# Kernel optimization log

Hardware: AMD Instinct MI355X
Metric: run time of the kernel (lower is better)

The kernel has to match this reference:

```python
import jax, jax.numpy as jnp
import numpy as np

NUM_HEADS = 8
LN_EPS = 1e-6


def _layer_norm(x, gamma, beta):
    mu = jnp.mean(x, axis=-1, keepdims=True)
    var = jnp.mean(jnp.square(x - mu), axis=-1, keepdims=True)
    return (x - mu) / jnp.sqrt(var + LN_EPS) * gamma + beta


def setup_inputs() -> dict:
    key = jax.random.key(0)
    B, S, H, F = 4, 2048, 1024, 4096
    ks = jax.random.split(key, 12)
    scale = 1.0 / np.sqrt(H)
    x = jax.random.normal(ks[0], (B, S, H), dtype=jnp.float32)
    # additive padding mask: 1 where masked, 0 where attended
    mask = jax.random.randint(ks[1], (B, 1, 1, S), 0, 2).astype(jnp.float32)
    Wq = jax.random.normal(ks[2], (H, H), dtype=jnp.float32) * scale
    Wk = jax.random.normal(ks[3], (H, H), dtype=jnp.float32) * scale
    Wv = jax.random.normal(ks[4], (H, H), dtype=jnp.float32) * scale
    Wo = jax.random.normal(ks[5], (H, H), dtype=jnp.float32) * scale
    W1 = jax.random.normal(ks[6], (H, F), dtype=jnp.float32) * scale
    b1 = jnp.zeros((F,), dtype=jnp.float32)
    W2 = jax.random.normal(ks[7], (F, H), dtype=jnp.float32) * (1.0 / np.sqrt(F))
    b2 = jnp.zeros((H,), dtype=jnp.float32)
    gamma = jnp.ones((H,), dtype=jnp.float32)
    beta = jnp.zeros((H,), dtype=jnp.float32)
    return {"x": x, "mask": mask, "Wq": Wq, "Wk": Wk, "Wv": Wv, "Wo": Wo,
            "W1": W1, "b1": b1, "W2": W2, "b2": b2, "gamma": gamma, "beta": beta}


def reference(x, mask, Wq, Wk, Wv, Wo, W1, b1, W2, b2, gamma, beta):
    B, S, H = x.shape
    nh = NUM_HEADS
    d = H // nh

    def split_heads(t):
        return t.reshape(B, S, nh, d).transpose(0, 2, 1, 3)  # [B,nh,S,d]

    q = split_heads(x @ Wq)
    k = split_heads(x @ Wk)
    v = split_heads(x @ Wv)

    # FAITHFUL to source bug: score /= d**(-0.5)  ==  score * sqrt(d)
    scores = jnp.einsum('bhqd,bhkd->bhqk', q, k) * jnp.sqrt(jnp.float32(d))
    scores = scores + mask * (-1e9)
    attn = jax.nn.softmax(scores, axis=-1)
    ctx = jnp.einsum('bhqk,bhkd->bhqd', attn, v)
    ctx = ctx.transpose(0, 2, 1, 3).reshape(B, S, H)
    attn_out = ctx @ Wo

    # dropout = identity (eval mode)
    x = _layer_norm(x + attn_out, gamma, beta)
    ffn = jnp.maximum(x @ W1 + b1, 0.0) @ W2 + b2
    x = _layer_norm(x + ffn, gamma, beta)
    return x
```

## Files before the change

kernel.cpp:

```cpp
#include <hip/hip_runtime.h>


typedef __bf16 bf16;
typedef __bf16 bf16x4 __attribute__((ext_vector_type(4)));
typedef __bf16 bf16x8 __attribute__((ext_vector_type(8)));
typedef float  f32x4  __attribute__((ext_vector_type(4)));

#define MFMA16(a, b, c) __builtin_amdgcn_mfma_f32_16x16x32_bf16(a, b, c, 0, 0, 0)

typedef const __attribute__((address_space(1))) void* gas_cptr;
typedef __attribute__((address_space(3))) void* las_ptr;

__device__ __forceinline__ void g2l16(const void* g, void* l) {
    __builtin_amdgcn_global_load_lds((gas_cptr)g, (las_ptr)l, 16, 0, 0);
}

__device__ __forceinline__ uint b16bits(bf16 v) {
    union { bf16 h; unsigned short u; } cv; cv.h = v; return (uint)cv.u;
}

__device__ __forceinline__ int xcd_swz(int d, int nwg) {
    return (d & 7) * (nwg >> 3) + (d >> 3);
}

__global__ __launch_bounds__(256) void split_f32_k(
    const float* __restrict__ in, bf16* __restrict__ hi, bf16* __restrict__ lo)
{
    const long i = (long)blockIdx.x * 256 + threadIdx.x;
    const float4 v = *(const float4*)(in + i * 4);
    const float a[4] = {v.x, v.y, v.z, v.w};
    bf16x4 h, l;
#pragma unroll
    for (int j = 0; j < 4; j++) {
        h[j] = (bf16)a[j];
        l[j] = (bf16)(a[j] - (float)h[j]);
    }
    *(bf16x4*)(hi + i * 4) = h;
    *(bf16x4*)(lo + i * 4) = l;
}

__global__ __launch_bounds__(256) void mask_scan_k(
    const float* __restrict__ mask, unsigned short* __restrict__ cidx,
    int* __restrict__ nbuf)
{
    __shared__ int wsum[4];
    const int b = blockIdx.x, t = threadIdx.x;
    const int lane = t & 63, w = t >> 6;
    float m[8];
    *(float4*)&m[0] = *(const float4*)(mask + b * 2048 + t * 8);
    *(float4*)&m[4] = *(const float4*)(mask + b * 2048 + t * 8 + 4);
    int keep[8], cnt = 0;
#pragma unroll
    for (int j = 0; j < 8; j++) {
        keep[j] = (m[j] < 0.5f) ? 1 : 0;
        cnt += keep[j];
    }
    int pre = cnt;
#pragma unroll
    for (int off = 1; off < 64; off <<= 1) {
        const int nv = __shfl_up(pre, off);
        if (lane >= off) pre += nv;
    }
    if (lane == 63) wsum[w] = pre;
    __syncthreads();
    int base = 0;
    for (int i = 0; i < w; i++) base += wsum[i];
    const int total = wsum[0] + wsum[1] + wsum[2] + wsum[3];
    int p = base + pre - cnt;
#pragma unroll
    for (int j = 0; j < 8; j++)
        if (keep[j]) cidx[b * 2048 + (p++)] = (unsigned short)(t * 8 + j);
    for (int j = t; j < 2048; j += 256)
        if (j >= total) cidx[b * 2048 + j] = 0;
    if (t == 0) nbuf[b] = total;
}

__global__ __launch_bounds__(256) void transpose_f32_k(
    const float* __restrict__ in, bf16* __restrict__ out_hi, bf16* __restrict__ out_lo,
    int in_rs, int out_rs)
{
    __shared__ uint Th[64][33];
    __shared__ uint Tl[64][33];
    const long c0 = (long)blockIdx.x * 64;
    const long r0 = (long)blockIdx.y * 64;
    const int t = threadIdx.x, rp = t >> 3, cc = t & 7;
    const float* pa = in + (r0 + 2 * rp) * (long)in_rs + c0 + cc * 8;
    const float* pb = pa + in_rs;
    float a[8], b[8];
    *(float4*)&a[0] = *(const float4*)pa;
    *(float4*)&a[4] = *(const float4*)(pa + 4);
    *(float4*)&b[0] = *(const float4*)pb;
    *(float4*)&b[4] = *(const float4*)(pb + 4);
#pragma unroll
    for (int j = 0; j < 8; j++) {
        const bf16 ah = (bf16)a[j], bh = (bf16)b[j];
        Th[cc * 8 + j][rp] = b16bits(ah) | (b16bits(bh) << 16);
        const bf16 al = (bf16)(a[j] - (float)ah), bl = (bf16)(b[j] - (float)bh);
        Tl[cc * 8 + j][rp] = b16bits(al) | (b16bits(bl) << 16);
    }
    __syncthreads();
#pragma unroll
    for (int i = 0; i < 2; i++) {
        const int task = i * 256 + t;
        const int c = task >> 3, ch = task & 7;
        uint4 wv;
        wv.x = Th[c][ch * 4 + 0]; wv.y = Th[c][ch * 4 + 1];
        wv.z = Th[c][ch * 4 + 2]; wv.w = Th[c][ch * 4 + 3];
        *(uint4*)(out_hi + (c0 + c) * (long)out_rs + r0 + ch * 8) = wv;
        if (out_lo) {
            uint4 wl;
            wl.x = Tl[c][ch * 4 + 0]; wl.y = Tl[c][ch * 4 + 1];
            wl.z = Tl[c][ch * 4 + 2]; wl.w = Tl[c][ch * 4 + 3];
            *(uint4*)(out_lo + (c0 + c) * (long)out_rs + r0 + ch * 8) = wl;
        }
    }
}

__global__ __launch_bounds__(256) void transpose_bf16_k(
    const bf16* __restrict__ in, bf16* __restrict__ out,
    int in_rs, int out_rs, int nh, long bo_in, long bi_in, long bo_out,
    const unsigned short* __restrict__ cidx, const int* __restrict__ nbuf)
{
    __shared__ uint T[64][33];
    const int z = blockIdx.z;
    const int bb = z / nh;
    const long r0 = (long)blockIdx.y * 64;
    if (nbuf) {
        const int npad = (nbuf[bb] + 63) & ~63;
        if (r0 >= npad) return;
    }
    const bf16* inp = in + (long)bb * bo_in + (long)(z % nh) * bi_in;
    bf16* outp = out + (long)z * bo_out;
    const long c0 = (long)blockIdx.x * 64;
    const int t = threadIdx.x, rp = t >> 3, cc = t & 7;

    long ra_i = r0 + 2 * rp, rb_i = ra_i + 1;
    if (cidx) {
        ra_i = cidx[bb * 2048 + ra_i];
        rb_i = cidx[bb * 2048 + rb_i];
    }
    const uint4 ra = *(const uint4*)(inp + ra_i * (long)in_rs + c0 + cc * 8);
    const uint4 rb = *(const uint4*)(inp + rb_i * (long)in_rs + c0 + cc * 8);
    const uint a32[4] = {ra.x, ra.y, ra.z, ra.w};
    const uint b32[4] = {rb.x, rb.y, rb.z, rb.w};
#pragma unroll
    for (int j = 0; j < 8; j++) {
        const uint av = (j & 1) ? (a32[j >> 1] >> 16) : (a32[j >> 1] & 0xffffu);
        const uint bv = (j & 1) ? (b32[j >> 1] >> 16) : (b32[j >> 1] & 0xffffu);
        T[cc * 8 + j][rp] = av | (bv << 16);
    }
    __syncthreads();
#pragma unroll
    for (int i = 0; i < 2; i++) {
        const int task = i * 256 + t;
        const int c = task >> 3, ch = task & 7;
        uint4 wv;
        wv.x = T[c][ch * 4 + 0]; wv.y = T[c][ch * 4 + 1];
        wv.z = T[c][ch * 4 + 2]; wv.w = T[c][ch * 4 + 3];
        *(uint4*)(outp + (c0 + c) * (long)out_rs + r0 + ch * 8) = wv;
    }
}

__global__ __launch_bounds__(256) void gemm_bf16_k(
    const bf16* __restrict__ A, const bf16* __restrict__ Bt,
    bf16* __restrict__ out,
    const float* __restrict__ bias, int relu, int M, int N, int K)
{
    __shared__ __align__(16) bf16 As[128 * 32];
    __shared__ __align__(16) bf16 Bs[128 * 32];
    const int t = threadIdx.x;
    const int fr = t & 15, fq = (t >> 4) & 3;
    const int w = t >> 6, wm = w & 1, wn = w >> 1;
    const int nx = gridDim.x;
    const int d = xcd_swz(blockIdx.y * nx + blockIdx.x, nx * gridDim.y);
    const long mBase = (long)(d / nx) * 128;
    const long nBase = (long)(d % nx) * 128;

    f32x4 acc[4][4];
#pragma unroll
    for (int i = 0; i < 4; i++)
#pragma unroll
        for (int j = 0; j < 4; j++) acc[i][j] = (f32x4){0.f, 0.f, 0.f, 0.f};

    const int arow = t >> 2;
    const int akc  = (t & 3) * 8;
    const bf16* ga0 = A + (mBase + arow) * (long)K + akc;
    const bf16* ga1 = A + (mBase + arow + 64) * (long)K + akc;
    const bf16* gb0 = Bt + (nBase + arow) * (long)K + akc;
    const bf16* gb1 = Bt + (nBase + arow + 64) * (long)K + akc;
    bf16* la0 = &As[t * 8];
    bf16* la1 = &As[(256 + t) * 8];
    bf16* lb0 = &Bs[t * 8];
    bf16* lb1 = &Bs[(256 + t) * 8];

    const int aoff = (wm * 64 + fr) * 32 + fq * 8;
    const int boff = (wn * 64 + fr) * 32 + fq * 8;

    for (int kt = 0; kt < K; kt += 32) {
        g2l16(ga0 + kt, la0);
        g2l16(ga1 + kt, la1);
        g2l16(gb0 + kt, lb0);
        g2l16(gb1 + kt, lb1);
        __syncthreads();
        bf16x8 af[4], bfv[4];
#pragma unroll
        for (int mt = 0; mt < 4; mt++) af[mt] = *(const bf16x8*)&As[aoff + mt * 512];
#pragma unroll
        for (int nt = 0; nt < 4; nt++) bfv[nt] = *(const bf16x8*)&Bs[boff + nt * 512];
#pragma unroll
        for (int mt = 0; mt < 4; mt++)
#pragma unroll
            for (int nt = 0; nt < 4; nt++)
                acc[mt][nt] = MFMA16(af[mt], bfv[nt], acc[mt][nt]);
        __syncthreads();
    }

    const long crow0 = mBase + wm * 64;
    const long ccol0 = nBase + wn * 64;
#pragma unroll
    for (int nt = 0; nt < 4; nt++) {
        const long col = ccol0 + nt * 16 + fr;
        const float bv = bias ? bias[col] : 0.0f;
#pragma unroll
        for (int mt = 0; mt < 4; mt++)
#pragma unroll
            for (int r = 0; r < 4; r++) {
                const long rowg = crow0 + mt * 16 + fq * 4 + r;
                float v = acc[mt][nt][r] + bv;
                if (relu) v = fmaxf(v, 0.0f);
                out[rowg * (long)N + col] = (bf16)v;
            }
    }
}

__global__ __launch_bounds__(256) void gemm_split_k(
    const bf16* __restrict__ Ah, const bf16* __restrict__ Al,
    const bf16* __restrict__ Bh, const bf16* __restrict__ Bl,
    bf16* __restrict__ out_hi, bf16* __restrict__ out_lo, int M, int N, int K)
{
    __shared__ __align__(16) bf16 Ahs[128 * 32];
    __shared__ __align__(16) bf16 Als[128 * 32];
    __shared__ __align__(16) bf16 Bhs[128 * 32];
    __shared__ __align__(16) bf16 Bls[128 * 32];
    const int t = threadIdx.x;
    const int fr = t & 15, fq = (t >> 4) & 3;
    const int w = t >> 6, wm = w & 1, wn = w >> 1;
    const int nx = gridDim.x;
    const int d = xcd_swz(blockIdx.y * nx + blockIdx.x, nx * gridDim.y);
    const long mBase = (long)(d / nx) * 128;
    const long nBase = (long)(d % nx) * 128;

    f32x4 acc[4][4];
#pragma unroll
    for (int i = 0; i < 4; i++)
#pragma unroll
        for (int j = 0; j < 4; j++) acc[i][j] = (f32x4){0.f, 0.f, 0.f, 0.f};

    const int arow = t >> 2;
    const int akc  = (t & 3) * 8;
    const long ga0 = (mBase + arow) * (long)K + akc;
    const long ga1 = (mBase + arow + 64) * (long)K + akc;
    const long gb0 = (nBase + arow) * (long)K + akc;
    const long gb1 = (nBase + arow + 64) * (long)K + akc;

    const int aoff = (wm * 64 + fr) * 32 + fq * 8;
    const int boff = (wn * 64 + fr) * 32 + fq * 8;

    for (int kt = 0; kt < K; kt += 32) {
        g2l16(Ah + ga0 + kt, &Ahs[t * 8]);
        g2l16(Ah + ga1 + kt, &Ahs[(256 + t) * 8]);
        g2l16(Al + ga0 + kt, &Als[t * 8]);
        g2l16(Al + ga1 + kt, &Als[(256 + t) * 8]);
        g2l16(Bh + gb0 + kt, &Bhs[t * 8]);
        g2l16(Bh + gb1 + kt, &Bhs[(256 + t) * 8]);
        g2l16(Bl + gb0 + kt, &Bls[t * 8]);
        g2l16(Bl + gb1 + kt, &Bls[(256 + t) * 8]);
        __syncthreads();
        bf16x8 ah[4], al[4], bh[4], bl[4];
#pragma unroll
        for (int mt = 0; mt < 4; mt++) {
            ah[mt] = *(const bf16x8*)&Ahs[aoff + mt * 512];
            al[mt] = *(const bf16x8*)&Als[aoff + mt * 512];
        }
#pragma unroll
        for (int nt = 0; nt < 4; nt++) {
            bh[nt] = *(const bf16x8*)&Bhs[boff + nt * 512];
            bl[nt] = *(const bf16x8*)&Bls[boff + nt * 512];
        }
#pragma unroll
        for (int mt = 0; mt < 4; mt++)
#pragma unroll
            for (int nt = 0; nt < 4; nt++) {
                acc[mt][nt] = MFMA16(ah[mt], bh[nt], acc[mt][nt]);
                acc[mt][nt] = MFMA16(ah[mt], bl[nt], acc[mt][nt]);
                acc[mt][nt] = MFMA16(al[mt], bh[nt], acc[mt][nt]);
            }
        __syncthreads();
    }

    const long crow0 = mBase + wm * 64;
    const long ccol0 = nBase + wn * 64;
#pragma unroll
    for (int nt = 0; nt < 4; nt++) {
        const long col = ccol0 + nt * 16 + fr;
#pragma unroll
        for (int mt = 0; mt < 4; mt++)
#pragma unroll
            for (int r = 0; r < 4; r++) {
                const long rowg = crow0 + mt * 16 + fq * 4 + r;
                const float v = acc[mt][nt][r];
                const long idx = rowg * (long)N + col;
                const bf16 h = (bf16)v;
                out_hi[idx] = h;
                out_lo[idx] = (bf16)(v - (float)h);
            }
    }
}

#define KROW 132
#define VROW 68
#define PROW 68
__global__ __launch_bounds__(256, 2) void flash_attn_k(
    const bf16* __restrict__ qhi, const bf16* __restrict__ qlo,
    const bf16* __restrict__ khi, const bf16* __restrict__ klo,
    const bf16* __restrict__ vt,
    const unsigned short* __restrict__ cidx, const int* __restrict__ nbuf,
    bf16* __restrict__ ctx)
{
    __shared__ __align__(16) bf16 Kh[64 * KROW];
    __shared__ __align__(16) bf16 Kl[64 * KROW];
    __shared__ __align__(16) bf16 Vs[128 * VROW];
    __shared__ __align__(16) bf16 Ps[4][16 * PROW];
    __shared__ __align__(16) unsigned short CI[2048];
    const float scale = 11.3137085f;
    const int t = threadIdx.x, w = t >> 6;
    const int fr = t & 15, fq = (t >> 4) & 3;
    const int blk = xcd_swz(blockIdx.x, 512);
    const int qt = blk & 15, bh_ = blk >> 4, b = bh_ >> 3, h = bh_ & 7;
    const int qrow0 = qt * 128 + w * 16;

    const int nB = nbuf[b];
    const int ntiles = (nB + 63) >> 6;
    *(uint4*)&CI[t * 8] = *(const uint4*)(cidx + (long)b * 2048 + t * 8);

    bf16x8 qh[2][4], ql[2][4];
#pragma unroll
    for (int mt = 0; mt < 2; mt++) {
        const long qoff = ((long)(b * 2048 + qrow0 + mt * 64 + fr)) * 1024 + h * 128 + fq * 8;
#pragma unroll
        for (int s = 0; s < 4; s++) {
            qh[mt][s] = *(const bf16x8*)(qhi + qoff + s * 32);
            ql[mt][s] = *(const bf16x8*)(qlo + qoff + s * 32);
        }
    }
    f32x4 o[2][8];
#pragma unroll
    for (int mt = 0; mt < 2; mt++)
#pragma unroll
        for (int nt = 0; nt < 8; nt++) o[mt][nt] = (f32x4){0.f, 0.f, 0.f, 0.f};
    float m_run[2][4], l_run[2][4];
#pragma unroll
    for (int mt = 0; mt < 2; mt++)
#pragma unroll
        for (int r = 0; r < 4; r++) { m_run[mt][r] = -1e30f; l_run[mt][r] = 0.f; }

    const long kbase = (long)(b * 2048) * 1024 + h * 128 + (long)(t & 15) * 8;
    const long vbase = ((long)bh_ * 128) * 2048 + (long)(t & 7) * 8;

    for (int kt = 0; kt < ntiles; kt++) {
        __syncthreads();
#pragma unroll
        for (int i = 0; i < 4; i++) {
            const int key = i * 16 + (t >> 4);
            const int srow = CI[kt * 64 + key];
            const long g = kbase + (long)srow * 1024;
            const bf16x8 vk_h = *(const bf16x8*)(khi + g);
            const bf16x8 vk_l = *(const bf16x8*)(klo + g);
            const int d = i * 32 + (t >> 3);
            const bf16x8 vv = *(const bf16x8*)(vt + vbase + (long)d * 2048 + kt * 64);
            *(bf16x8*)&Kh[key * KROW + (t & 15) * 8] = vk_h;
            *(bf16x8*)&Kl[key * KROW + (t & 15) * 8] = vk_l;
            *(bf16x8*)&Vs[d * VROW + (t & 7) * 8] = vv;
        }
        float madd[4];
#pragma unroll
        for (int ct = 0; ct < 4; ct++)
            madd[ct] = (kt * 64 + ct * 16 + fr < nB) ? 0.0f : -1e9f;
        __syncthreads();

        f32x4 sc[2][4];
#pragma unroll
        for (int mt = 0; mt < 2; mt++)
#pragma unroll
            for (int ct = 0; ct < 4; ct++) sc[mt][ct] = (f32x4){0.f, 0.f, 0.f, 0.f};
        __builtin_amdgcn_s_setprio(1);
#pragma unroll
        for (int s = 0; s < 4; s++)
#pragma unroll
            for (int ct = 0; ct < 4; ct++) {
                const int off = (ct * 16 + fr) * KROW + s * 32 + fq * 8;
                const bf16x8 kh8 = *(const bf16x8*)&Kh[off];
                const bf16x8 kl8 = *(const bf16x8*)&Kl[off];
#pragma unroll
                for (int mt = 0; mt < 2; mt++) {
                    sc[mt][ct] = MFMA16(qh[mt][s], kh8, sc[mt][ct]);
                    sc[mt][ct] = MFMA16(qh[mt][s], kl8, sc[mt][ct]);
                    sc[mt][ct] = MFMA16(ql[mt][s], kh8, sc[mt][ct]);
                }
            }
        __builtin_amdgcn_s_setprio(0);

#pragma unroll
        for (int mt = 0; mt < 2; mt++) {
            float alpha[4];
#pragma unroll
            for (int r = 0; r < 4; r++) {
                float mx = sc[mt][0][r] * scale + madd[0];
                mx = fmaxf(mx, sc[mt][1][r] * scale + madd[1]);
                mx = fmaxf(mx, sc[mt][2][r] * scale + madd[2]);
                mx = fmaxf(mx, sc[mt][3][r] * scale + madd[3]);
                mx = fmaxf(mx, __shfl_xor(mx, 1));
                mx = fmaxf(mx, __shfl_xor(mx, 2));
                mx = fmaxf(mx, __shfl_xor(mx, 4));
                mx = fmaxf(mx, __shfl_xor(mx, 8));
                const float mn = fmaxf(m_run[mt][r], mx);
                alpha[r] = __expf(m_run[mt][r] - mn);
                m_run[mt][r] = mn;
            }
            float lt[4] = {0.f, 0.f, 0.f, 0.f};
#pragma unroll
            for (int ct = 0; ct < 4; ct++)
#pragma unroll
                for (int r = 0; r < 4; r++) {
                    const float p = __expf(sc[mt][ct][r] * scale + madd[ct] - m_run[mt][r]);
                    lt[r] += p;
                    Ps[w][(fq * 4 + r) * PROW + ct * 16 + fr] = (bf16)p;
                }
#pragma unroll
            for (int r = 0; r < 4; r++) {
                float s_ = lt[r];
                s_ += __shfl_xor(s_, 1); s_ += __shfl_xor(s_, 2);
                s_ += __shfl_xor(s_, 4); s_ += __shfl_xor(s_, 8);
                l_run[mt][r] = l_run[mt][r] * alpha[r] + s_;
            }
            const int need = (alpha[0] < 1.f) | (alpha[1] < 1.f) |
                             (alpha[2] < 1.f) | (alpha[3] < 1.f);
            if (__any(need)) {
#pragma unroll
                for (int nt = 0; nt < 8; nt++)
#pragma unroll
                    for (int r = 0; r < 4; r++) o[mt][nt][r] *= alpha[r];
            }

            __builtin_amdgcn_s_setprio(1);
#pragma unroll
            for (int sp = 0; sp < 2; sp++) {
                const bf16x8 pf = *(const bf16x8*)&Ps[w][fr * PROW + sp * 32 + fq * 8];
#pragma unroll
                for (int nt = 0; nt < 8; nt++) {
                    const bf16x8 vf = *(const bf16x8*)&Vs[(nt * 16 + fr) * VROW + sp * 32 + fq * 8];
                    o[mt][nt] = MFMA16(pf, vf, o[mt][nt]);
                }
            }
            __builtin_amdgcn_s_setprio(0);
        }
    }
#pragma unroll
    for (int mt = 0; mt < 2; mt++)
#pragma unroll
        for (int r = 0; r < 4; r++) {
            const float inv = l_run[mt][r] > 0.f ? 1.0f / l_run[mt][r] : 0.f;
#pragma unroll
            for (int nt = 0; nt < 8; nt++) {
                const long idx = ((long)(b * 2048 + qrow0 + mt * 64 + fq * 4 + r)) * 1024
                               + h * 128 + nt * 16 + fr;
                ctx[idx] = (bf16)(o[mt][nt][r] * inv);
            }
        }
}

__global__ __launch_bounds__(256) void add_ln_k(
    const float* __restrict__ xf, const bf16* __restrict__ y,
    const float* __restrict__ gamma, const float* __restrict__ beta,
    float* __restrict__ out, bf16* __restrict__ out_b)
{
    __shared__ float red[8];
    const long row = blockIdx.x;
    const int t = threadIdx.x, lane = t & 63, w = t >> 6;
    float v[4];
    const float4 xv = *(const float4*)(xf + row * 1024 + t * 4);
    v[0] = xv.x; v[1] = xv.y; v[2] = xv.z; v[3] = xv.w;
    const bf16x4 yv = *(const bf16x4*)(y + row * 1024 + t * 4);
    float s = 0.f, s2 = 0.f;
#pragma unroll
    for (int i = 0; i < 4; i++) {
        v[i] += (float)yv[i];
        s += v[i]; s2 += v[i] * v[i];
    }
#pragma unroll
    for (int off = 1; off < 64; off <<= 1) {
        s += __shfl_xor(s, off);
        s2 += __shfl_xor(s2, off);
    }
    if (lane == 0) { red[w] = s; red[4 + w] = s2; }
    __syncthreads();
    s = red[0] + red[1] + red[2] + red[3];
    s2 = red[4] + red[5] + red[6] + red[7];
    const float mean = s * (1.0f / 1024.0f);
    const float var = s2 * (1.0f / 1024.0f) - mean * mean;
    const float rstd = rsqrtf(var + 1e-6f);
    float4 ov;
    ov.x = (v[0] - mean) * rstd * gamma[t * 4 + 0] + beta[t * 4 + 0];
    ov.y = (v[1] - mean) * rstd * gamma[t * 4 + 1] + beta[t * 4 + 1];
    ov.z = (v[2] - mean) * rstd * gamma[t * 4 + 2] + beta[t * 4 + 2];
    ov.w = (v[3] - mean) * rstd * gamma[t * 4 + 3] + beta[t * 4 + 3];
    *(float4*)(out + row * 1024 + t * 4) = ov;
    if (out_b) {
        bf16x4 hb;
        hb[0] = (bf16)ov.x; hb[1] = (bf16)ov.y; hb[2] = (bf16)ov.z; hb[3] = (bf16)ov.w;
        *(bf16x4*)(out_b + row * 1024 + t * 4) = hb;
    }
}

extern "C" void kernel_launch(void* const* d_in, const int* in_sizes, int n_in,
                              void* d_out, int out_size, void* d_ws, size_t ws_size,
                              hipStream_t stream)
{
    (void)in_sizes; (void)n_in; (void)out_size; (void)ws_size;
    const float* x     = (const float*)d_in[0];
    const float* mask  = (const float*)d_in[1];
    const float* Wq    = (const float*)d_in[2];
    const float* Wk    = (const float*)d_in[3];
    const float* Wv    = (const float*)d_in[4];
    const float* Wo    = (const float*)d_in[5];
    const float* W1    = (const float*)d_in[6];
    const float* b1    = (const float*)d_in[7];
    const float* W2    = (const float*)d_in[8];
    const float* b2    = (const float*)d_in[9];
    const float* gamma = (const float*)d_in[10];
    const float* beta  = (const float*)d_in[11];
    float* out = (float*)d_out;

    char* ws = (char*)d_ws;
    const size_t SZ = 8192ul * 1024 * 2;
    bf16* qhi  = (bf16*)(ws + 0 * SZ);
    bf16* qlo  = (bf16*)(ws + 1 * SZ);
    bf16* khi  = (bf16*)(ws + 2 * SZ);
    bf16* klo  = (bf16*)(ws + 3 * SZ);
    bf16* hbuf = (bf16*)(ws + 0 * SZ);
    bf16* vbuf = (bf16*)(ws + 4 * SZ);
    bf16* ctxb = vbuf;
    bf16* vtb  = (bf16*)(ws + 5 * SZ);
    bf16* fbuf = vtb;
    bf16* xh   = (bf16*)(ws + 6 * SZ);
    bf16* xl   = (bf16*)(ws + 7 * SZ);
    bf16* aob  = xl;
    float* x1f = (float*)(ws + 8 * SZ);
    bf16* x1b  = (bf16*)(ws + 10 * SZ);
    char* wts  = ws + 11 * SZ;
    bf16* Wqth = (bf16*)(wts);
    bf16* Wqtl = (bf16*)(wts + 1 * 2097152);
    bf16* Wkth = (bf16*)(wts + 2 * 2097152);
    bf16* Wktl = (bf16*)(wts + 3 * 2097152);
    bf16* Wvt  = (bf16*)(wts + 4 * 2097152);
    bf16* Wot  = (bf16*)(wts + 5 * 2097152);
    bf16* W1t  = (bf16*)(wts + 6 * 2097152);
    bf16* W2t  = (bf16*)(wts + 6 * 2097152 + 8388608);
    unsigned short* cidxb = (unsigned short*)(wts + 6 * 2097152 + 2 * 8388608);
    int* nbuf = (int*)((char*)cidxb + 4 * 2048 * sizeof(unsigned short));

    const dim3 blk(256);
    split_f32_k<<<dim3(8192), blk, 0, stream>>>(x, xh, xl);
    mask_scan_k<<<dim3(4), blk, 0, stream>>>(mask, cidxb, nbuf);
    transpose_f32_k<<<dim3(16, 16), blk, 0, stream>>>(Wq, Wqth, Wqtl, 1024, 1024);
    transpose_f32_k<<<dim3(16, 16), blk, 0, stream>>>(Wk, Wkth, Wktl, 1024, 1024);
    transpose_f32_k<<<dim3(16, 16), blk, 0, stream>>>(Wv, Wvt, nullptr, 1024, 1024);
    transpose_f32_k<<<dim3(16, 16), blk, 0, stream>>>(Wo, Wot, nullptr, 1024, 1024);
    transpose_f32_k<<<dim3(64, 16), blk, 0, stream>>>(W1, W1t, nullptr, 4096, 1024);
    transpose_f32_k<<<dim3(16, 64), blk, 0, stream>>>(W2, W2t, nullptr, 1024, 4096);
    gemm_split_k<<<dim3(8, 64), blk, 0, stream>>>(xh, xl, Wqth, Wqtl, qhi, qlo, 8192, 1024, 1024);
    gemm_split_k<<<dim3(8, 64), blk, 0, stream>>>(xh, xl, Wkth, Wktl, khi, klo, 8192, 1024, 1024);
    gemm_bf16_k<<<dim3(8, 64), blk, 0, stream>>>(xh, Wvt, vbuf, nullptr, 0, 8192, 1024, 1024);
    transpose_bf16_k<<<dim3(2, 32, 32), blk, 0, stream>>>(vbuf, vtb, 1024, 2048, 8,
                                                          (long)2048 * 1024, 128L, (long)128 * 2048,
                                                          cidxb, nbuf);
    flash_attn_k<<<dim3(512), blk, 0, stream>>>(qhi, qlo, khi, klo, vtb, cidxb, nbuf, ctxb);
    gemm_bf16_k<<<dim3(8, 64), blk, 0, stream>>>(ctxb, Wot, aob, nullptr, 0, 8192, 1024, 1024);
    add_ln_k<<<dim3(8192), blk, 0, stream>>>(x, aob, gamma, beta, x1f, x1b);
    gemm_bf16_k<<<dim3(32, 64), blk, 0, stream>>>(x1b, W1t, hbuf, b1, 1, 8192, 4096, 1024);
    gemm_bf16_k<<<dim3(8, 64), blk, 0, stream>>>(hbuf, W2t, fbuf, b2, 0, 8192, 1024, 4096);
    add_ln_k<<<dim3(8192), blk, 0, stream>>>(x1f, fbuf, gamma, beta, out, nullptr);
}
```

Before: 662.9 us.

## Compact unmasked keys inside K/V projection GEMMs and skip padded row tiles

The K and V projection GEMMs now gather only the unmasked key rows through the compaction index and write them densely. Row tiles past the padded count of valid keys exit early. Attention and the V transpose then read contiguous compacted rows instead of gathering through the index per tile. This cuts about half of the K and V projection work under a random padding mask and removes the indirect loads in attention. In exchange the GEMM A loads become row gathers, and the compacted buffer tail beyond the valid count is left stale, which relies on the existing -1e9 masking in attention.

```diff
diff --git a/kernel.cpp b/kernel.cpp
--- a/kernel.cpp
+++ b/kernel.cpp
@@ -119,7 +119,7 @@
 __global__ __launch_bounds__(256) void transpose_bf16_k(
     const bf16* __restrict__ in, bf16* __restrict__ out,
     int in_rs, int out_rs, int nh, long bo_in, long bi_in, long bo_out,
-    const unsigned short* __restrict__ cidx, const int* __restrict__ nbuf)
+    const int* __restrict__ nbuf)
 {
     __shared__ uint T[64][33];
     const int z = blockIdx.z;
@@ -134,13 +134,8 @@
     const long c0 = (long)blockIdx.x * 64;
     const int t = threadIdx.x, rp = t >> 3, cc = t & 7;
 
-    long ra_i = r0 + 2 * rp, rb_i = ra_i + 1;
-    if (cidx) {
-        ra_i = cidx[bb * 2048 + ra_i];
-        rb_i = cidx[bb * 2048 + rb_i];
-    }
-    const uint4 ra = *(const uint4*)(inp + ra_i * (long)in_rs + c0 + cc * 8);
-    const uint4 rb = *(const uint4*)(inp + rb_i * (long)in_rs + c0 + cc * 8);
+    const uint4 ra = *(const uint4*)(inp + (r0 + 2 * rp) * (long)in_rs + c0 + cc * 8);
+    const uint4 rb = *(const uint4*)(inp + (r0 + 2 * rp + 1) * (long)in_rs + c0 + cc * 8);
     const uint a32[4] = {ra.x, ra.y, ra.z, ra.w};
     const uint b32[4] = {rb.x, rb.y, rb.z, rb.w};
 #pragma unroll
@@ -164,7 +159,8 @@
 __global__ __launch_bounds__(256) void gemm_bf16_k(
     const bf16* __restrict__ A, const bf16* __restrict__ Bt,
     bf16* __restrict__ out,
-    const float* __restrict__ bias, int relu, int M, int N, int K)
+    const float* __restrict__ bias, int relu, int M, int N, int K,
+    const unsigned short* __restrict__ cidx, const int* __restrict__ nbuf)
 {
     __shared__ __align__(16) bf16 As[128 * 32];
     __shared__ __align__(16) bf16 Bs[128 * 32];
@@ -176,16 +172,25 @@
     const long mBase = (long)(d / nx) * 128;
     const long nBase = (long)(d % nx) * 128;
 
-    f32x4 acc[4][4];
-#pragma unroll
-    for (int i = 0; i < 4; i++)
-#pragma unroll
-        for (int j = 0; j < 4; j++) acc[i][j] = (f32x4){0.f, 0.f, 0.f, 0.f};
-
     const int arow = t >> 2;
     const int akc  = (t & 3) * 8;
-    const bf16* ga0 = A + (mBase + arow) * (long)K + akc;
-    const bf16* ga1 = A + (mBase + arow + 64) * (long)K + akc;
+    long r0 = mBase + arow, r1 = r0 + 64;
+    if (cidx) {
+        const int b = (int)(mBase >> 11);
+        const int npad = (nbuf[b] + 63) & ~63;
+        if ((int)(mBase & 2047) >= npad) return;
+        r0 = (long)b * 2048 + cidx[b * 2048 + (int)(r0 & 2047)];
+        r1 = (long)b * 2048 + cidx[b * 2048 + (int)(r1 & 2047)];
+    }
+
+    f32x4 acc[4][4];
+#pragma unroll
+    for (int i = 0; i < 4; i++)
+#pragma unroll
+        for (int j = 0; j < 4; j++) acc[i][j] = (f32x4){0.f, 0.f, 0.f, 0.f};
+
+    const bf16* ga0 = A + r0 * (long)K + akc;
+    const bf16* ga1 = A + r1 * (long)K + akc;
     const bf16* gb0 = Bt + (nBase + arow) * (long)K + akc;
     const bf16* gb1 = Bt + (nBase + arow + 64) * (long)K + akc;
     bf16* la0 = &As[t * 8];
@@ -236,7 +241,8 @@
 __global__ __launch_bounds__(256) void gemm_split_k(
     const bf16* __restrict__ Ah, const bf16* __restrict__ Al,
     const bf16* __restrict__ Bh, const bf16* __restrict__ Bl,
-    bf16* __restrict__ out_hi, bf16* __restrict__ out_lo, int M, int N, int K)
+    bf16* __restrict__ out_hi, bf16* __restrict__ out_lo, int M, int N, int K,
+    const unsigned short* __restrict__ cidx, const int* __restrict__ nbuf)
 {
     __shared__ __align__(16) bf16 Ahs[128 * 32];
     __shared__ __align__(16) bf16 Als[128 * 32];
@@ -250,16 +256,25 @@
     const long mBase = (long)(d / nx) * 128;
     const long nBase = (long)(d % nx) * 128;
 
-    f32x4 acc[4][4];
-#pragma unroll
-    for (int i = 0; i < 4; i++)
-#pragma unroll
-        for (int j = 0; j < 4; j++) acc[i][j] = (f32x4){0.f, 0.f, 0.f, 0.f};
-
     const int arow = t >> 2;
     const int akc  = (t & 3) * 8;
-    const long ga0 = (mBase + arow) * (long)K + akc;
-    const long ga1 = (mBase + arow + 64) * (long)K + akc;
+    long r0 = mBase + arow, r1 = r0 + 64;
+    if (cidx) {
+        const int b = (int)(mBase >> 11);
+        const int npad = (nbuf[b] + 63) & ~63;
+        if ((int)(mBase & 2047) >= npad) return;
+        r0 = (long)b * 2048 + cidx[b * 2048 + (int)(r0 & 2047)];
+        r1 = (long)b * 2048 + cidx[b * 2048 + (int)(r1 & 2047)];
+    }
+
+    f32x4 acc[4][4];
+#pragma unroll
+    for (int i = 0; i < 4; i++)
+#pragma unroll
+        for (int j = 0; j < 4; j++) acc[i][j] = (f32x4){0.f, 0.f, 0.f, 0.f};
+
+    const long ga0 = r0 * (long)K + akc;
+    const long ga1 = r1 * (long)K + akc;
     const long gb0 = (nBase + arow) * (long)K + akc;
     const long gb1 = (nBase + arow + 64) * (long)K + akc;
 
@@ -323,15 +338,13 @@
 __global__ __launch_bounds__(256, 2) void flash_attn_k(
     const bf16* __restrict__ qhi, const bf16* __restrict__ qlo,
     const bf16* __restrict__ khi, const bf16* __restrict__ klo,
-    const bf16* __restrict__ vt,
-    const unsigned short* __restrict__ cidx, const int* __restrict__ nbuf,
+    const bf16* __restrict__ vt, const int* __restrict__ nbuf,
     bf16* __restrict__ ctx)
 {
     __shared__ __align__(16) bf16 Kh[64 * KROW];
     __shared__ __align__(16) bf16 Kl[64 * KROW];
     __shared__ __align__(16) bf16 Vs[128 * VROW];
     __shared__ __align__(16) bf16 Ps[4][16 * PROW];
-    __shared__ __align__(16) unsigned short CI[2048];
     const float scale = 11.3137085f;
     const int t = threadIdx.x, w = t >> 6;
     const int fr = t & 15, fq = (t >> 4) & 3;
@@ -341,7 +354,6 @@
 
     const int nB = nbuf[b];
     const int ntiles = (nB + 63) >> 6;
-    *(uint4*)&CI[t * 8] = *(const uint4*)(cidx + (long)b * 2048 + t * 8);
 
     bf16x8 qh[2][4], ql[2][4];
 #pragma unroll
@@ -372,8 +384,7 @@
 #pragma unroll
         for (int i = 0; i < 4; i++) {
             const int key = i * 16 + (t >> 4);
-            const int srow = CI[kt * 64 + key];
-            const long g = kbase + (long)srow * 1024;
+            const long g = kbase + (long)(kt * 64 + key) * 1024;
             const bf16x8 vk_h = *(const bf16x8*)(khi + g);
             const bf16x8 vk_l = *(const bf16x8*)(klo + g);
             const int d = i * 32 + (t >> 3);
@@ -578,16 +589,22 @@
     transpose_f32_k<<<dim3(16, 16), blk, 0, stream>>>(Wo, Wot, nullptr, 1024, 1024);
     transpose_f32_k<<<dim3(64, 16), blk, 0, stream>>>(W1, W1t, nullptr, 4096, 1024);
     transpose_f32_k<<<dim3(16, 64), blk, 0, stream>>>(W2, W2t, nullptr, 1024, 4096);
-    gemm_split_k<<<dim3(8, 64), blk, 0, stream>>>(xh, xl, Wqth, Wqtl, qhi, qlo, 8192, 1024, 1024);
-    gemm_split_k<<<dim3(8, 64), blk, 0, stream>>>(xh, xl, Wkth, Wktl, khi, klo, 8192, 1024, 1024);
-    gemm_bf16_k<<<dim3(8, 64), blk, 0, stream>>>(xh, Wvt, vbuf, nullptr, 0, 8192, 1024, 1024);
+    gemm_split_k<<<dim3(8, 64), blk, 0, stream>>>(xh, xl, Wqth, Wqtl, qhi, qlo, 8192, 1024, 1024,
+                                                  nullptr, nullptr);
+    gemm_split_k<<<dim3(8, 64), blk, 0, stream>>>(xh, xl, Wkth, Wktl, khi, klo, 8192, 1024, 1024,
+                                                  cidxb, nbuf);
+    gemm_bf16_k<<<dim3(8, 64), blk, 0, stream>>>(xh, Wvt, vbuf, nullptr, 0, 8192, 1024, 1024,
+                                                 cidxb, nbuf);
     transpose_bf16_k<<<dim3(2, 32, 32), blk, 0, stream>>>(vbuf, vtb, 1024, 2048, 8,
                                                           (long)2048 * 1024, 128L, (long)128 * 2048,
-                                                          cidxb, nbuf);
-    flash_attn_k<<<dim3(512), blk, 0, stream>>>(qhi, qlo, khi, klo, vtb, cidxb, nbuf, ctxb);
-    gemm_bf16_k<<<dim3(8, 64), blk, 0, stream>>>(ctxb, Wot, aob, nullptr, 0, 8192, 1024, 1024);
+                                                          nbuf);
+    flash_attn_k<<<dim3(512), blk, 0, stream>>>(qhi, qlo, khi, klo, vtb, nbuf, ctxb);
+    gemm_bf16_k<<<dim3(8, 64), blk, 0, stream>>>(ctxb, Wot, aob, nullptr, 0, 8192, 1024, 1024,
+                                                 nullptr, nullptr);
     add_ln_k<<<dim3(8192), blk, 0, stream>>>(x, aob, gamma, beta, x1f, x1b);
-    gemm_bf16_k<<<dim3(32, 64), blk, 0, stream>>>(x1b, W1t, hbuf, b1, 1, 8192, 4096, 1024);
-    gemm_bf16_k<<<dim3(8, 64), blk, 0, stream>>>(hbuf, W2t, fbuf, b2, 0, 8192, 1024, 4096);
+    gemm_bf16_k<<<dim3(32, 64), blk, 0, stream>>>(x1b, W1t, hbuf, b1, 1, 8192, 4096, 1024,
+                                                  nullptr, nullptr);
+    gemm_bf16_k<<<dim3(8, 64), blk, 0, stream>>>(hbuf, W2t, fbuf, b2, 0, 8192, 1024, 4096,
+                                                 nullptr, nullptr);
     add_ln_k<<<dim3(8192), blk, 0, stream>>>(x1f, fbuf, gamma, beta, out, nullptr);
 }
```

New measurement: 661.1 us. About the same (-0.3%).
